# Performance work log

Measured on AMD Instinct MI355X. Metric: run time of the kernel, lower is better.

The kernel has to match this reference:

```python
import jax, jax.numpy as jnp
import numpy as np
import math

V, D, H, NL, L, B = 32000, 1024, 16, 6, 1024, 2
HD = D // H
EPS = 1e-5


def _positional(L, D):
    # matches torch: exp(arange(0,D,2) * -(log(1000)/D))
    div = jnp.exp(jnp.arange(0, D, 2, dtype=jnp.float32) * (-math.log(1000.0) / D))
    k = jnp.arange(L, dtype=jnp.float32)[:, None]
    pos = jnp.zeros((L, D), dtype=jnp.float32)
    pos = pos.at[:, 0::2].set(jnp.sin(k * div))
    pos = pos.at[:, 1::2].set(jnp.cos(k * div))
    return pos[None]  # [1, L, D]


def setup_inputs() -> dict:
    key = jax.random.key(0)
    ks = jax.random.split(key, 12)
    s = 0.02
    tokens = jax.random.randint(ks[0], (B, L), 0, V)
    emb = jax.random.normal(ks[1], (V, D), jnp.float32) * s
    pos = _positional(L, D)
    ln1_g = jnp.ones((NL, D), jnp.float32)
    ln1_b = jnp.zeros((NL, D), jnp.float32)
    ln2_g = jnp.ones((NL, D), jnp.float32)
    ln2_b = jnp.zeros((NL, D), jnp.float32)
    attn_w = jax.random.normal(ks[2], (NL, D, 3 * D), jnp.float32) * s
    attn_b = jnp.zeros((NL, 3 * D), jnp.float32)
    proj_w = jax.random.normal(ks[3], (NL, D, D), jnp.float32) * s
    proj_b = jnp.zeros((NL, D), jnp.float32)
    mlp_w1 = jax.random.normal(ks[4], (NL, D, 4 * D), jnp.float32) * s
    mlp_b1 = jnp.zeros((NL, 4 * D), jnp.float32)
    mlp_w2 = jax.random.normal(ks[5], (NL, 4 * D, D), jnp.float32) * s
    mlp_b2 = jnp.zeros((NL, D), jnp.float32)
    out_w = jax.random.normal(ks[6], (D, V), jnp.float32) * s
    return dict(tokens=tokens, pos=pos, emb=emb,
                ln1_g=ln1_g, ln1_b=ln1_b, ln2_g=ln2_g, ln2_b=ln2_b,
                attn_w=attn_w, attn_b=attn_b, proj_w=proj_w, proj_b=proj_b,
                mlp_w1=mlp_w1, mlp_b1=mlp_b1, mlp_w2=mlp_w2, mlp_b2=mlp_b2,
                out_w=out_w)


def _ln(x, g, b):
    mu = jnp.mean(x, -1, keepdims=True)
    var = jnp.mean(jnp.square(x - mu), -1, keepdims=True)
    return (x - mu) * jax.lax.rsqrt(var + EPS) * g + b


def _block(x, p, causal_mask):
    ln1_g, ln1_b, ln2_g, ln2_b, aw, ab, pw, pb, w1, b1, w2, b2 = p
    h = _ln(x, ln1_g, ln1_b)
    qkv = h @ aw + ab                      # [B, L, 3D]
    q, k, v = jnp.split(qkv, 3, axis=-1)
    Bc, Lc = x.shape[0], x.shape[1]
    q = q.reshape(Bc, Lc, H, HD)
    k = k.reshape(Bc, Lc, H, HD)
    v = v.reshape(Bc, Lc, H, HD)
    scores = jnp.einsum('blhd,bmhd->bhlm', q, k) * (1.0 / math.sqrt(HD))
    scores = jnp.where(causal_mask, scores, -jnp.inf)
    attn = jax.nn.softmax(scores, axis=-1)
    y = jnp.einsum('bhlm,bmhd->blhd', attn, v).reshape(Bc, Lc, D)
    x = x + (y @ pw + pb)
    r = _ln(x, ln2_g, ln2_b)
    # NOTE: original ModuleList order applies GELU AFTER the second linear
    r = jax.nn.gelu((r @ w1 + b1) @ w2 + b2, approximate=False)
    return x + r


def reference(tokens, pos, emb, ln1_g, ln1_b, ln2_g, ln2_b,
              attn_w, attn_b, proj_w, proj_b,
              mlp_w1, mlp_b1, mlp_w2, mlp_b2, out_w):
    x = emb[tokens] + pos                  # [B, L, D]
    Lc = x.shape[1]
    causal_mask = jnp.tril(jnp.ones((Lc, Lc), bool))[None, None]
    for i in range(NL):
        p = (ln1_g[i], ln1_b[i], ln2_g[i], ln2_b[i],
             attn_w[i], attn_b[i], proj_w[i], proj_b[i],
             mlp_w1[i], mlp_b1[i], mlp_w2[i], mlp_b2[i])
        x = _block(x, p, causal_mask)
    return x @ out_w                       # [B, L, V] logits
```

## Files before the change

### kernel.cpp

```cpp
#include <hip/hip_runtime.h>
#include <hip/hip_bf16.h>
#include <math.h>

typedef __bf16 bf16;
typedef __bf16 bf16x4 __attribute__((ext_vector_type(4)));
typedef __bf16 bf16x8 __attribute__((ext_vector_type(8)));
typedef float f32x4 __attribute__((ext_vector_type(4)));

__device__ __forceinline__ void gld_lds16(const void* g, void* l) {
    __builtin_amdgcn_global_load_lds(
        (const __attribute__((address_space(1))) unsigned int*)g,
        (__attribute__((address_space(3))) unsigned int*)l, 16, 0, 0);
}

#define VMW(n) asm volatile("s_waitcnt vmcnt(" #n ")" ::: "memory")
#define BARR() asm volatile("s_barrier" ::: "memory")

__global__ __launch_bounds__(256) void k_embed(const int* __restrict__ tok,
                                               const float* __restrict__ emb,
                                               const float* __restrict__ pos,
                                               float* __restrict__ x) {
    int row = blockIdx.x;
    int l = row & 1023;
    int tk = tok[row];
    const float4* e = (const float4*)(emb + (size_t)tk * 1024);
    const float4* p = (const float4*)(pos + (size_t)l * 1024);
    float4* o = (float4*)(x + (size_t)row * 1024);
    float4 a = e[threadIdx.x], b = p[threadIdx.x];
    o[threadIdx.x] = make_float4(a.x + b.x, a.y + b.y, a.z + b.z, a.w + b.w);
}

__global__ __launch_bounds__(256) void k_ln(const float* __restrict__ x,
                                            const float* __restrict__ g,
                                            const float* __restrict__ b,
                                            bf16* __restrict__ out) {
    int row = blockIdx.x;
    int t = threadIdx.x;
    const float4* xr = (const float4*)(x + (size_t)row * 1024);
    float4 v = xr[t];
    float s1 = v.x + v.y + v.z + v.w;
    float s2 = v.x * v.x + v.y * v.y + v.z * v.z + v.w * v.w;
#pragma unroll
    for (int o = 32; o; o >>= 1) { s1 += __shfl_down(s1, o); s2 += __shfl_down(s2, o); }
    __shared__ float ps1[4], ps2[4], stat[2];
    int lane = t & 63, wid = t >> 6;
    if (lane == 0) { ps1[wid] = s1; ps2[wid] = s2; }
    __syncthreads();
    if (t == 0) {
        float a1 = ps1[0] + ps1[1] + ps1[2] + ps1[3];
        float a2 = ps2[0] + ps2[1] + ps2[2] + ps2[3];
        float mu = a1 * (1.f / 1024.f);
        float var = a2 * (1.f / 1024.f) - mu * mu;
        stat[0] = mu; stat[1] = rsqrtf(var + 1e-5f);
    }
    __syncthreads();
    float mu = stat[0], rs = stat[1];
    const float4* gv = (const float4*)g;
    const float4* bv = (const float4*)b;
    float4 gg = gv[t], bb = bv[t];
    bf16x4 o4;
    o4[0] = (bf16)((v.x - mu) * rs * gg.x + bb.x);
    o4[1] = (bf16)((v.y - mu) * rs * gg.y + bb.y);
    o4[2] = (bf16)((v.z - mu) * rs * gg.z + bb.z);
    o4[3] = (bf16)((v.w - mu) * rs * gg.w + bb.w);
    *(bf16x4*)(out + (size_t)row * 1024 + t * 4) = o4;
}

__device__ __forceinline__ void transpose64(const float* __restrict__ W,
                                            bf16* __restrict__ WT,
                                            int K, int N, int n0, int k0, int t,
                                            float (*tile)[65]) {
    int tx = t & 15, ty = t >> 4;
#pragma unroll
    for (int i = 0; i < 64; i += 16) {
        float4 v = *(const float4*)&W[(size_t)(k0 + ty + i) * N + n0 + tx * 4];
        tile[ty + i][tx * 4 + 0] = v.x;
        tile[ty + i][tx * 4 + 1] = v.y;
        tile[ty + i][tx * 4 + 2] = v.z;
        tile[ty + i][tx * 4 + 3] = v.w;
    }
    __syncthreads();
    int n = t >> 3, ks = t & 7;
#pragma unroll
    for (int pass = 0; pass < 2; ++pass) {
        int nn = n + pass * 32;
        bf16x8 v;
#pragma unroll
        for (int j = 0; j < 8; ++j) v[j] = (bf16)tile[ks * 8 + j][nn];
        *(bf16x8*)&WT[(size_t)(n0 + nn) * K + k0 + ks * 8] = v;
    }
}

__device__ __forceinline__ void tr_layer_block(int bid,
                                               const float* aw, const float* pw,
                                               const float* m1, const float* m2,
                                               bf16* wT, int t, float (*tile)[65]) {
    const float* src; bf16* dst; int K, N, tn, tk;
    if (bid < 768)       { src = aw; dst = wT;            K = 1024; N = 3072; tn = bid % 48; tk = bid / 48; }
    else if (bid < 1024) { int b = bid - 768;  src = pw; dst = wT + 3145728; K = 1024; N = 1024; tn = b % 16; tk = b / 16; }
    else if (bid < 2048) { int b = bid - 1024; src = m1; dst = wT + 4194304; K = 1024; N = 4096; tn = b % 64; tk = b / 64; }
    else                 { int b = bid - 2048; src = m2; dst = wT + 8388608; K = 4096; N = 1024; tn = b % 16; tk = b / 16; }
    transpose64(src, dst, K, N, tn * 64, tk * 64, t, tile);
}

__global__ __launch_bounds__(256) void k_transpose_layer(const float* __restrict__ aw,
                                                         const float* __restrict__ pw,
                                                         const float* __restrict__ m1,
                                                         const float* __restrict__ m2,
                                                         bf16* __restrict__ wT) {
    __shared__ float tile[64][65];
    tr_layer_block(blockIdx.x, aw, pw, m1, m2, wT, threadIdx.x, tile);
}

__device__ __forceinline__ void stage128(const char* Ab, const char* Bb,
                                         char* As, char* Bs, int Kb, int k0b, int t) {
#pragma unroll
    for (int j = 0; j < 4; ++j) {
        int idx = j * 256 + t;
        int row = idx >> 3;
        int cb = (idx & 7) << 4;
        int scb = cb ^ ((row & 7) << 4);
        gld_lds16(Ab + (size_t)row * Kb + k0b + scb, As + idx * 16);
        gld_lds16(Bb + (size_t)row * Kb + k0b + scb, Bs + idx * 16);
    }
}

template <int EPI>
__global__ __launch_bounds__(256) void k_gemm2(const bf16* __restrict__ A,
                                               const bf16* __restrict__ BT,
                                               const float* __restrict__ bias,
                                               const float* __restrict__ resid,
                                               float* __restrict__ outf,
                                               bf16* __restrict__ outb,
                                               int N, int K) {
    __shared__ __align__(16) bf16 As[2][128 * 64];
    __shared__ __align__(16) bf16 Bs[2][128 * 64];
    int per = gridDim.x >> 3;
    int tile = (blockIdx.x & 7) * per + (blockIdx.x >> 3);
    int bm = tile & 15, bn = tile >> 4;
    int t = threadIdx.x, lane = t & 63;
    int wr = t >> 7, wc = (t >> 6) & 1;
    f32x4 acc[4][4] = {};
    const char* Ab = (const char*)(A + (size_t)bm * 128 * K);
    const char* Bb = (const char*)(BT + (size_t)bn * 128 * K);
    int Kb = K * 2;
    int nk = K >> 6;
    stage128(Ab, Bb, (char*)As[0], (char*)Bs[0], Kb, 0, t);
    VMW(0); BARR();
    for (int tt = 0; tt < nk; ++tt) {
        int cur = tt & 1;
        if (tt + 1 < nk)
            stage128(Ab, Bb, (char*)As[cur ^ 1], (char*)Bs[cur ^ 1], Kb, (tt + 1) * 128, t);
        const char* Ac = (const char*)As[cur];
        const char* Bc = (const char*)Bs[cur];
#pragma unroll
        for (int kk = 0; kk < 2; ++kk) {
            bf16x8 af[4], bfr[4];
            int cb = kk * 64 + ((lane >> 4) << 4);
#pragma unroll
            for (int m = 0; m < 4; ++m) {
                int r = wr * 64 + m * 16 + (lane & 15);
                af[m] = *(const bf16x8*)(Ac + r * 128 + (cb ^ ((r & 7) << 4)));
            }
#pragma unroll
            for (int n = 0; n < 4; ++n) {
                int r = wc * 64 + n * 16 + (lane & 15);
                bfr[n] = *(const bf16x8*)(Bc + r * 128 + (cb ^ ((r & 7) << 4)));
            }
#pragma unroll
            for (int m = 0; m < 4; ++m)
#pragma unroll
                for (int n = 0; n < 4; ++n)
                    acc[m][n] = __builtin_amdgcn_mfma_f32_16x16x32_bf16(af[m], bfr[n], acc[m][n], 0, 0, 0);
        }
        VMW(0); BARR();
    }
    int row0 = bm * 128 + wr * 64 + ((lane >> 4) << 2);
    int col0 = bn * 128 + wc * 64 + (lane & 15);
#pragma unroll
    for (int m = 0; m < 4; ++m) {
#pragma unroll
        for (int n = 0; n < 4; ++n) {
            int col = col0 + n * 16;
            float bv = bias[col];
#pragma unroll
            for (int r = 0; r < 4; ++r) {
                int row = row0 + m * 16 + r;
                size_t idx = (size_t)row * N + col;
                float v = acc[m][n][r] + bv;
                if (EPI == 0) {
                    outb[idx] = (bf16)v;
                } else if (EPI == 1) {
                    outf[idx] = resid[idx] + v;
                } else {
                    outf[idx] = resid[idx] + 0.5f * v * (1.0f + erff(v * 0.70710678118f));
                }
            }
        }
    }
}

__device__ __forceinline__ void stage64(const char* Ab, const char* Bb,
                                        char* As, char* Bs, int Kb, int k0b, int t) {
#pragma unroll
    for (int j = 0; j < 2; ++j) {
        int idx = j * 256 + t;
        int row = idx >> 3;
        int cb = (idx & 7) << 4;
        int scb = cb ^ ((row & 7) << 4);
        gld_lds16(Ab + (size_t)row * Kb + k0b + scb, As + idx * 16);
        gld_lds16(Bb + (size_t)row * Kb + k0b + scb, Bs + idx * 16);
    }
}

template <int EPI>
__global__ __launch_bounds__(256) void k_gemm64(const bf16* __restrict__ A,
                                                const bf16* __restrict__ BT,
                                                const float* __restrict__ bias,
                                                const float* __restrict__ resid,
                                                float* __restrict__ outf,
                                                bf16* __restrict__ outb,
                                                int N, int K) {
    __shared__ __align__(16) bf16 As[2][64 * 64];
    __shared__ __align__(16) bf16 Bs[2][64 * 64];
    int per = gridDim.x >> 3;
    int tile = (blockIdx.x & 7) * per + (blockIdx.x >> 3);
    int bm = tile & 31, bn = tile >> 5;
    int t = threadIdx.x, lane = t & 63, wid = t >> 6;
    f32x4 acc[4] = {};
    const char* Ab = (const char*)(A + (size_t)bm * 64 * K);
    const char* Bb = (const char*)(BT + (size_t)bn * 64 * K);
    int Kb = K * 2;
    int nk = K >> 6;
    stage64(Ab, Bb, (char*)As[0], (char*)Bs[0], Kb, 0, t);
    VMW(0); BARR();
    for (int tt = 0; tt < nk; ++tt) {
        int cur = tt & 1;
        if (tt + 1 < nk)
            stage64(Ab, Bb, (char*)As[cur ^ 1], (char*)Bs[cur ^ 1], Kb, (tt + 1) * 128, t);
        const char* Ac = (const char*)As[cur];
        const char* Bc = (const char*)Bs[cur];
#pragma unroll
        for (int kk = 0; kk < 2; ++kk) {
            int cb = kk * 64 + ((lane >> 4) << 4);
            int ra = wid * 16 + (lane & 15);
            bf16x8 af = *(const bf16x8*)(Ac + ra * 128 + (cb ^ ((ra & 7) << 4)));
            bf16x8 bfr[4];
#pragma unroll
            for (int n = 0; n < 4; ++n) {
                int r = n * 16 + (lane & 15);
                bfr[n] = *(const bf16x8*)(Bc + r * 128 + (cb ^ ((r & 7) << 4)));
            }
#pragma unroll
            for (int n = 0; n < 4; ++n)
                acc[n] = __builtin_amdgcn_mfma_f32_16x16x32_bf16(af, bfr[n], acc[n], 0, 0, 0);
        }
        VMW(0); BARR();
    }
    int row0 = bm * 64 + wid * 16 + ((lane >> 4) << 2);
    int col0 = bn * 64 + (lane & 15);
#pragma unroll
    for (int n = 0; n < 4; ++n) {
        int col = col0 + n * 16;
        float bv = bias[col];
#pragma unroll
        for (int r = 0; r < 4; ++r) {
            int row = row0 + r;
            size_t idx = (size_t)row * N + col;
            float v = acc[n][r] + bv;
            float res;
            if (EPI == 1) {
                res = resid[idx] + v;
            } else {
                res = resid[idx] + 0.5f * v * (1.0f + erff(v * 0.70710678118f));
            }
            outf[idx] = res;
            if (outb) outb[idx] = (bf16)res;
        }
    }
}

__device__ __forceinline__ void stage_full256(const char* gtile, char* ldst,
                                              int Kb, int t) {
#pragma unroll
    for (int j = 0; j < 4; ++j) {
        int idx = j * 512 + t;
        int row = idx >> 3;
        int cb = (idx & 7) << 4;
        int scb = cb ^ ((row & 7) << 4);
        gld_lds16(gtile + (size_t)row * Kb + scb, ldst + idx * 16);
    }
}

__device__ __forceinline__ void stage_half256(const char* gtile, char* ldst,
                                              int Kb, int t, int half) {
#pragma unroll
    for (int j = 0; j < 2; ++j) {
        int idx = (half * 2 + j) * 512 + t;
        int row = idx >> 3;
        int cb = (idx & 7) << 4;
        int scb = cb ^ ((row & 7) << 4);
        gld_lds16(gtile + (size_t)row * Kb + scb, ldst + idx * 16);
    }
}

template <int MH, int NH>
__device__ __forceinline__ void phase_rd(const char* Ac, const char* Bc,
                                         int lrow, int lk, int wm, int wn,
                                         bf16x8 (&af)[4][2], bf16x8 (&bfr)[2][2]) {
#pragma unroll
    for (int kk = 0; kk < 2; ++kk) {
        int cb = kk * 64 + lk * 16;
#pragma unroll
        for (int m = 0; m < 4; ++m) {
            int row = (MH * 4 + m) * 32 + wm * 16 + lrow;
            af[m][kk] = *(const bf16x8*)(Ac + row * 128 + (cb ^ ((row & 7) << 4)));
        }
#pragma unroll
        for (int n = 0; n < 2; ++n) {
            int row = (NH * 2 + n) * 64 + wn * 16 + lrow;
            bfr[n][kk] = *(const bf16x8*)(Bc + row * 128 + (cb ^ ((row & 7) << 4)));
        }
    }
}

template <int MH, int NH>
__device__ __forceinline__ void phase_mm(bf16x8 (&af)[4][2], bf16x8 (&bfr)[2][2],
                                         f32x4 (&acc)[8][4]) {
    __builtin_amdgcn_s_setprio(1);
#pragma unroll
    for (int kk = 0; kk < 2; ++kk)
#pragma unroll
        for (int m = 0; m < 4; ++m)
#pragma unroll
            for (int n = 0; n < 2; ++n)
                acc[MH * 4 + m][NH * 2 + n] = __builtin_amdgcn_mfma_f32_16x16x32_bf16(
                    af[m][kk], bfr[n][kk], acc[MH * 4 + m][NH * 2 + n], 0, 0, 0);
    __builtin_amdgcn_s_setprio(0);
    __builtin_amdgcn_sched_barrier(0);
}

__global__ __launch_bounds__(512, 1) void k_gemm256(const bf16* __restrict__ A,
                                                    const bf16* __restrict__ BT,
                                                    float* __restrict__ outf,
                                                    int N, int K) {
    __shared__ __align__(16) bf16 Asb[2][256 * 64];
    __shared__ __align__(16) bf16 Bsb[3][256 * 64];
    int t = threadIdx.x, lane = t & 63, wid = t >> 6;
    int wm = wid >> 2, wn = wid & 3;
    int lrow = lane & 15, lk = lane >> 4;
    int tile = (blockIdx.x & 7) * 125 + (blockIdx.x >> 3);
    int bm = tile & 7;
    int bn = tile >> 3;

    const char* Ab = (const char*)(A + (size_t)bm * 256 * K);
    const char* Bb = (const char*)(BT + (size_t)bn * 256 * K);
    int Kb = K * 2;
    int nk = K >> 6;
    f32x4 acc[8][4] = {};

    stage_full256(Ab, (char*)Asb[0], Kb, t);
    stage_full256(Bb, (char*)Bsb[0], Kb, t);
    stage_full256(Bb + 128, (char*)Bsb[1], Kb, t);

    for (int tt = 0; tt < nk; ++tt) {
        int ka = (tt + 1 < nk) ? tt + 1 : nk - 1;
        int kb = (tt + 2 < nk) ? tt + 2 : nk - 1;
        const char* Ac = (const char*)Asb[tt & 1];
        const char* Bc = (const char*)Bsb[tt % 3];
        char* An = (char*)Asb[(tt + 1) & 1];
        char* Bn = (char*)Bsb[(tt + 2) % 3];
        const char* Ag = Ab + (size_t)ka * 128;
        const char* Bg = Bb + (size_t)kb * 128;
        VMW(4); BARR();
        bf16x8 af[4][2], bfr[2][2];
        phase_rd<0, 0>(Ac, Bc, lrow, lk, wm, wn, af, bfr);
        stage_half256(Ag, An, Kb, t, 0);
        BARR();
        phase_mm<0, 0>(af, bfr, acc);
        BARR();
        phase_rd<0, 1>(Ac, Bc, lrow, lk, wm, wn, af, bfr);
        stage_half256(Ag, An, Kb, t, 1);
        BARR();
        phase_mm<0, 1>(af, bfr, acc);
        BARR();
        phase_rd<1, 0>(Ac, Bc, lrow, lk, wm, wn, af, bfr);
        stage_half256(Bg, Bn, Kb, t, 0);
        BARR();
        phase_mm<1, 0>(af, bfr, acc);
        BARR();
        phase_rd<1, 1>(Ac, Bc, lrow, lk, wm, wn, af, bfr);
        stage_half256(Bg, Bn, Kb, t, 1);
        BARR();
        phase_mm<1, 1>(af, bfr, acc);
        BARR();
    }

    size_t row0 = (size_t)bm * 256 + wm * 16 + (lane >> 4) * 4;
    int col0 = bn * 256 + wn * 16 + (lane & 15);
#pragma unroll
    for (int mi = 0; mi < 8; ++mi) {
#pragma unroll
        for (int ni = 0; ni < 4; ++ni) {
            int col = col0 + ni * 64;
#pragma unroll
            for (int r = 0; r < 4; ++r) {
                size_t row = row0 + mi * 32 + r;
                outf[row * N + col] = acc[mi][ni][r];
            }
        }
    }
}

__global__ __launch_bounds__(256) void k_attn_tr(const bf16* __restrict__ qkv,
                                                 bf16* __restrict__ y,
                                                 const float* __restrict__ aw,
                                                 const float* __restrict__ pw,
                                                 const float* __restrict__ m1,
                                                 const float* __restrict__ m2,
                                                 bf16* __restrict__ wTnext,
                                                 const float* __restrict__ outw,
                                                 bf16* __restrict__ outT) {
    __shared__ __align__(16) char smem[32768];
    int bidg = blockIdx.x;
    int t = threadIdx.x;
    if (bidg >= 512) {
        int tb = bidg - 512;
        float (*tile)[65] = (float(*)[65])smem;
        if (aw) {
            tr_layer_block(tb, aw, pw, m1, m2, wTnext, t, tile);
        } else {
            int tn = tb % 500, tk = tb / 500;
            transpose64(outw, outT, 1024, 32000, tn * 64, tk * 64, t, tile);
        }
        return;
    }
    bf16* Qs = (bf16*)smem;
    bf16* Ks = Qs + 4096;
    bf16* Vt = Ks + 4096;
    bf16* Ps = Vt + 4096;
    int tile = (bidg & 7) * 64 + (bidg >> 3);
    int qb = tile & 15;
    int bh = tile >> 4;
    int b = bh >> 4, h = bh & 15;
    int lane = t & 63, wid = t >> 6;
    int lr = lane & 15, lk = lane >> 4;
    int tok0 = b << 10;
    int q0 = qb << 6;
    const char* qbase = (const char*)qkv;
#pragma unroll
    for (int j = 0; j < 2; ++j) {
        int off = (j * 256 + t) * 16;
        int row = off >> 7, colb = off & 127;
        int scb = colb ^ ((row & 7) << 4);
        gld_lds16(qbase + ((size_t)(tok0 + q0 + row) * 3072 + h * 64) * 2 + scb, (char*)Qs + off);
    }
    VMW(0);
    __syncthreads();
    int qrw = wid * 16 + lr;
    int qsw = (qrw & 7) << 4;
    bf16x8 aq0 = *(const bf16x8*)((const char*)Qs + qrw * 128 + ((lk * 16) ^ qsw));
    bf16x8 aq1 = *(const bf16x8*)((const char*)Qs + qrw * 128 + ((64 + lk * 16) ^ qsw));
    f32x4 o[4] = {};
    float mrun[4], lrun[4];
#pragma unroll
    for (int r = 0; r < 4; ++r) { mrun[r] = -INFINITY; lrun[r] = 0.f; }
    int qrow = q0 + wid * 16 + lk * 4;

    for (int kv0 = 0; kv0 <= q0; kv0 += 64) {
        __syncthreads();
#pragma unroll
        for (int j = 0; j < 2; ++j) {
            int off = (j * 256 + t) * 16;
            int row = off >> 7, colb = off & 127;
            int scb = colb ^ ((row & 7) << 4);
            gld_lds16(qbase + ((size_t)(tok0 + kv0 + row) * 3072 + 1024 + h * 64) * 2 + scb,
                      (char*)Ks + off);
        }
        {
            int kv = t >> 2, d0 = (t & 3) * 16;
            const bf16* vrow = qkv + (size_t)(tok0 + kv0 + kv) * 3072 + 2048 + h * 64 + d0;
#pragma unroll
            for (int e4 = 0; e4 < 4; ++e4) {
                bf16x4 vv = *(const bf16x4*)(vrow + e4 * 4);
#pragma unroll
                for (int i = 0; i < 4; ++i) {
                    int d = d0 + e4 * 4 + i;
                    Vt[d * 64 + (kv ^ ((d & 7) << 3))] = vv[i];
                }
            }
        }
        VMW(0);
        __syncthreads();
        f32x4 s[4];
#pragma unroll
        for (int n = 0; n < 4; ++n) {
            int krw = n * 16 + lr;
            int ksw = (krw & 7) << 4;
            const char* kb = (const char*)Ks + krw * 128;
            bf16x8 bk0 = *(const bf16x8*)(kb + ((lk * 16) ^ ksw));
            bf16x8 bk1 = *(const bf16x8*)(kb + ((64 + lk * 16) ^ ksw));
            f32x4 z = {};
            z = __builtin_amdgcn_mfma_f32_16x16x32_bf16(aq0, bk0, z, 0, 0, 0);
            z = __builtin_amdgcn_mfma_f32_16x16x32_bf16(aq1, bk1, z, 0, 0, 0);
            s[n] = z;
        }
        float mx[4];
#pragma unroll
        for (int r = 0; r < 4; ++r) mx[r] = -INFINITY;
#pragma unroll
        for (int n = 0; n < 4; ++n) {
            int col = kv0 + n * 16 + lr;
#pragma unroll
            for (int r = 0; r < 4; ++r) {
                float sv = s[n][r] * 0.125f;
                sv = (col <= qrow + r) ? sv : -INFINITY;
                s[n][r] = sv;
                mx[r] = fmaxf(mx[r], sv);
            }
        }
#pragma unroll
        for (int r = 0; r < 4; ++r)
#pragma unroll
            for (int m = 1; m < 16; m <<= 1) mx[r] = fmaxf(mx[r], __shfl_xor(mx[r], m));
        float scl[4];
#pragma unroll
        for (int r = 0; r < 4; ++r) {
            float mn = fmaxf(mrun[r], mx[r]);
            scl[r] = __expf(mrun[r] - mn);
            mrun[r] = mn;
        }
        float rs[4] = {0.f, 0.f, 0.f, 0.f};
#pragma unroll
        for (int n = 0; n < 4; ++n)
#pragma unroll
            for (int r = 0; r < 4; ++r) {
                float p = __expf(s[n][r] - mrun[r]);
                s[n][r] = p;
                rs[r] += p;
            }
#pragma unroll
        for (int r = 0; r < 4; ++r) {
#pragma unroll
            for (int m = 1; m < 16; m <<= 1) rs[r] += __shfl_xor(rs[r], m);
            lrun[r] = lrun[r] * scl[r] + rs[r];
        }
#pragma unroll
        for (int n = 0; n < 4; ++n)
#pragma unroll
            for (int r = 0; r < 4; ++r) {
                o[n][r] *= scl[r];
                int prow = lk * 4 + r;
                Ps[wid * 1024 + prow * 64 + ((n * 16 + lr) ^ ((prow & 7) << 3))] = (bf16)s[n][r];
            }
        int psw = (lr & 7) << 3;
        const bf16* pb = Ps + wid * 1024 + lr * 64;
        bf16x8 ap0 = *(const bf16x8*)(pb + ((lk * 8) ^ psw));
        bf16x8 ap1 = *(const bf16x8*)(pb + ((32 + lk * 8) ^ psw));
#pragma unroll
        for (int n = 0; n < 4; ++n) {
            int vrw = n * 16 + lr;
            int vsw = (vrw & 7) << 3;
            const bf16* vb = Vt + vrw * 64;
            bf16x8 bv0 = *(const bf16x8*)(vb + ((lk * 8) ^ vsw));
            bf16x8 bv1 = *(const bf16x8*)(vb + ((32 + lk * 8) ^ vsw));
            o[n] = __builtin_amdgcn_mfma_f32_16x16x32_bf16(ap0, bv0, o[n], 0, 0, 0);
            o[n] = __builtin_amdgcn_mfma_f32_16x16x32_bf16(ap1, bv1, o[n], 0, 0, 0);
        }
    }
#pragma unroll
    for (int n = 0; n < 4; ++n)
#pragma unroll
        for (int r = 0; r < 4; ++r) {
            int row = tok0 + qrow + r;
            y[(size_t)row * 1024 + h * 64 + n * 16 + lr] = (bf16)(o[n][r] / lrun[r]);
        }
}

extern "C" void kernel_launch(void* const* d_in, const int* in_sizes, int n_in,
                              void* d_out, int out_size, void* d_ws, size_t ws_size,
                              hipStream_t stream) {
    const int*   tokens = (const int*)d_in[0];
    const float* pos    = (const float*)d_in[1];
    const float* emb    = (const float*)d_in[2];
    const float* ln1_g  = (const float*)d_in[3];
    const float* ln1_b  = (const float*)d_in[4];
    const float* ln2_g  = (const float*)d_in[5];
    const float* ln2_b  = (const float*)d_in[6];
    const float* attn_w = (const float*)d_in[7];
    const float* attn_b = (const float*)d_in[8];
    const float* proj_w = (const float*)d_in[9];
    const float* proj_b = (const float*)d_in[10];
    const float* mlp_w1 = (const float*)d_in[11];
    const float* mlp_b1 = (const float*)d_in[12];
    const float* mlp_w2 = (const float*)d_in[13];
    const float* mlp_b2 = (const float*)d_in[14];
    const float* out_w  = (const float*)d_in[15];
    float* out = (float*)d_out;

    char* ws = (char*)d_ws;
    size_t off = 0;
    auto alloc = [&](size_t bytes) {
        void* p = ws + off;
        off = (off + bytes + 255) & ~(size_t)255;
        return p;
    };
    float* x   = (float*)alloc((size_t)2048 * 1024 * 4);
    bf16* hb   = (bf16*)alloc((size_t)2048 * 1024 * 2);
    bf16* qkvb = (bf16*)alloc((size_t)2048 * 3072 * 2);
    bf16* yb   = (bf16*)alloc((size_t)2048 * 1024 * 2);
    bf16* hidb = (bf16*)alloc((size_t)2048 * 4096 * 2);
    bf16* outT = (bf16*)alloc((size_t)32000 * 1024 * 2);
    bf16* slot1 = (bf16*)alloc((size_t)9437184 * 2);
    bf16* slots[2] = { outT, slot1 };

    k_embed<<<2048, 256, 0, stream>>>(tokens, emb, pos, x);
    k_transpose_layer<<<3072, 256, 0, stream>>>(attn_w, proj_w, mlp_w1, mlp_w2, slots[0]);

    for (int i = 0; i < 6; ++i) {
        bf16* wT = slots[i & 1];
        k_ln<<<2048, 256, 0, stream>>>(x, ln1_g + i * 1024, ln1_b + i * 1024, hb);
        k_gemm2<0><<<384, 256, 0, stream>>>(hb, wT, attn_b + i * 3072,
                                            nullptr, nullptr, qkvb, 3072, 1024);
        if (i < 5) {
            int j = i + 1;
            k_attn_tr<<<3584, 256, 0, stream>>>(qkvb, yb,
                attn_w + (size_t)j * 1024 * 3072, proj_w + (size_t)j * 1024 * 1024,
                mlp_w1 + (size_t)j * 1024 * 4096, mlp_w2 + (size_t)j * 4096 * 1024,
                slots[j & 1], nullptr, nullptr);
        } else {
            k_attn_tr<<<8512, 256, 0, stream>>>(qkvb, yb,
                nullptr, nullptr, nullptr, nullptr, nullptr, out_w, outT);
        }
        k_gemm64<1><<<512, 256, 0, stream>>>(yb, wT + 3145728, proj_b + i * 1024,
                                             x, x, nullptr, 1024, 1024);
        k_ln<<<2048, 256, 0, stream>>>(x, ln2_g + i * 1024, ln2_b + i * 1024, hb);
        k_gemm2<0><<<512, 256, 0, stream>>>(hb, wT + 4194304, mlp_b1 + i * 4096,
                                            nullptr, nullptr, hidb, 4096, 1024);
        k_gemm64<2><<<512, 256, 0, stream>>>(hidb, wT + 8388608, mlp_b2 + i * 1024,
                                             x, x, (i == 5) ? hb : nullptr, 1024, 4096);
    }

    k_gemm256<<<1000, 512, 0, stream>>>(hb, outT, out, 32000, 1024);
}
```

Measured before the change: 1.137 ms.

## Replace 256-tile LM-head GEMM with 128-tile kernel and QKV with 64-tile GEMM

Removes the hand-pipelined 256x256 k_gemm256 kernel and computes the final vocab projection with the generic 128x128 k_gemm2, using a new no-bias fp32-output epilogue. The QKV projection moves from the 128-tile GEMM to the 64-tile GEMM, which gains a bf16-output epilogue, so it launches more blocks. This trades the LM head's larger tile and better operand reuse for simpler code, and gives the QKV GEMM more parallelism across CUs at the cost of more operand reloads.

```diff
diff --git a/kernel.cpp b/kernel.cpp
--- a/kernel.cpp
+++ b/kernel.cpp
@@ -182,7 +182,7 @@
 #pragma unroll
         for (int n = 0; n < 4; ++n) {
             int col = col0 + n * 16;
-            float bv = bias[col];
+            float bv = (EPI == 3) ? 0.f : bias[col];
 #pragma unroll
             for (int r = 0; r < 4; ++r) {
                 int row = row0 + m * 16 + r;
@@ -192,8 +192,10 @@
                     outb[idx] = (bf16)v;
                 } else if (EPI == 1) {
                     outf[idx] = resid[idx] + v;
+                } else if (EPI == 2) {
+                    outf[idx] = resid[idx] + 0.5f * v * (1.0f + erff(v * 0.70710678118f));
                 } else {
-                    outf[idx] = resid[idx] + 0.5f * v * (1.0f + erff(v * 0.70710678118f));
+                    outf[idx] = v;
                 }
             }
         }
@@ -268,145 +270,17 @@
             int row = row0 + r;
             size_t idx = (size_t)row * N + col;
             float v = acc[n][r] + bv;
-            float res;
-            if (EPI == 1) {
-                res = resid[idx] + v;
+            if (EPI == 0) {
+                outb[idx] = (bf16)v;
             } else {
-                res = resid[idx] + 0.5f * v * (1.0f + erff(v * 0.70710678118f));
-            }
-            outf[idx] = res;
-            if (outb) outb[idx] = (bf16)res;
-        }
-    }
-}
-
-__device__ __forceinline__ void stage_full256(const char* gtile, char* ldst,
-                                              int Kb, int t) {
-#pragma unroll
-    for (int j = 0; j < 4; ++j) {
-        int idx = j * 512 + t;
-        int row = idx >> 3;
-        int cb = (idx & 7) << 4;
-        int scb = cb ^ ((row & 7) << 4);
-        gld_lds16(gtile + (size_t)row * Kb + scb, ldst + idx * 16);
-    }
-}
-
-__device__ __forceinline__ void stage_half256(const char* gtile, char* ldst,
-                                              int Kb, int t, int half) {
-#pragma unroll
-    for (int j = 0; j < 2; ++j) {
-        int idx = (half * 2 + j) * 512 + t;
-        int row = idx >> 3;
-        int cb = (idx & 7) << 4;
-        int scb = cb ^ ((row & 7) << 4);
-        gld_lds16(gtile + (size_t)row * Kb + scb, ldst + idx * 16);
-    }
-}
-
-template <int MH, int NH>
-__device__ __forceinline__ void phase_rd(const char* Ac, const char* Bc,
-                                         int lrow, int lk, int wm, int wn,
-                                         bf16x8 (&af)[4][2], bf16x8 (&bfr)[2][2]) {
-#pragma unroll
-    for (int kk = 0; kk < 2; ++kk) {
-        int cb = kk * 64 + lk * 16;
-#pragma unroll
-        for (int m = 0; m < 4; ++m) {
-            int row = (MH * 4 + m) * 32 + wm * 16 + lrow;
-            af[m][kk] = *(const bf16x8*)(Ac + row * 128 + (cb ^ ((row & 7) << 4)));
-        }
-#pragma unroll
-        for (int n = 0; n < 2; ++n) {
-            int row = (NH * 2 + n) * 64 + wn * 16 + lrow;
-            bfr[n][kk] = *(const bf16x8*)(Bc + row * 128 + (cb ^ ((row & 7) << 4)));
-        }
-    }
-}
-
-template <int MH, int NH>
-__device__ __forceinline__ void phase_mm(bf16x8 (&af)[4][2], bf16x8 (&bfr)[2][2],
-                                         f32x4 (&acc)[8][4]) {
-    __builtin_amdgcn_s_setprio(1);
-#pragma unroll
-    for (int kk = 0; kk < 2; ++kk)
-#pragma unroll
-        for (int m = 0; m < 4; ++m)
-#pragma unroll
-            for (int n = 0; n < 2; ++n)
-                acc[MH * 4 + m][NH * 2 + n] = __builtin_amdgcn_mfma_f32_16x16x32_bf16(
-                    af[m][kk], bfr[n][kk], acc[MH * 4 + m][NH * 2 + n], 0, 0, 0);
-    __builtin_amdgcn_s_setprio(0);
-    __builtin_amdgcn_sched_barrier(0);
-}
-
-__global__ __launch_bounds__(512, 1) void k_gemm256(const bf16* __restrict__ A,
-                                                    const bf16* __restrict__ BT,
-                                                    float* __restrict__ outf,
-                                                    int N, int K) {
-    __shared__ __align__(16) bf16 Asb[2][256 * 64];
-    __shared__ __align__(16) bf16 Bsb[3][256 * 64];
-    int t = threadIdx.x, lane = t & 63, wid = t >> 6;
-    int wm = wid >> 2, wn = wid & 3;
-    int lrow = lane & 15, lk = lane >> 4;
-    int tile = (blockIdx.x & 7) * 125 + (blockIdx.x >> 3);
-    int bm = tile & 7;
-    int bn = tile >> 3;
-
-    const char* Ab = (const char*)(A + (size_t)bm * 256 * K);
-    const char* Bb = (const char*)(BT + (size_t)bn * 256 * K);
-    int Kb = K * 2;
-    int nk = K >> 6;
-    f32x4 acc[8][4] = {};
-
-    stage_full256(Ab, (char*)Asb[0], Kb, t);
-    stage_full256(Bb, (char*)Bsb[0], Kb, t);
-    stage_full256(Bb + 128, (char*)Bsb[1], Kb, t);
-
-    for (int tt = 0; tt < nk; ++tt) {
-        int ka = (tt + 1 < nk) ? tt + 1 : nk - 1;
-        int kb = (tt + 2 < nk) ? tt + 2 : nk - 1;
-        const char* Ac = (const char*)Asb[tt & 1];
-        const char* Bc = (const char*)Bsb[tt % 3];
-        char* An = (char*)Asb[(tt + 1) & 1];
-        char* Bn = (char*)Bsb[(tt + 2) % 3];
-        const char* Ag = Ab + (size_t)ka * 128;
-        const char* Bg = Bb + (size_t)kb * 128;
-        VMW(4); BARR();
-        bf16x8 af[4][2], bfr[2][2];
-        phase_rd<0, 0>(Ac, Bc, lrow, lk, wm, wn, af, bfr);
-        stage_half256(Ag, An, Kb, t, 0);
-        BARR();
-        phase_mm<0, 0>(af, bfr, acc);
-        BARR();
-        phase_rd<0, 1>(Ac, Bc, lrow, lk, wm, wn, af, bfr);
-        stage_half256(Ag, An, Kb, t, 1);
-        BARR();
-        phase_mm<0, 1>(af, bfr, acc);
-        BARR();
-        phase_rd<1, 0>(Ac, Bc, lrow, lk, wm, wn, af, bfr);
-        stage_half256(Bg, Bn, Kb, t, 0);
-        BARR();
-        phase_mm<1, 0>(af, bfr, acc);
-        BARR();
-        phase_rd<1, 1>(Ac, Bc, lrow, lk, wm, wn, af, bfr);
-        stage_half256(Bg, Bn, Kb, t, 1);
-        BARR();
-        phase_mm<1, 1>(af, bfr, acc);
-        BARR();
-    }
-
-    size_t row0 = (size_t)bm * 256 + wm * 16 + (lane >> 4) * 4;
-    int col0 = bn * 256 + wn * 16 + (lane & 15);
-#pragma unroll
-    for (int mi = 0; mi < 8; ++mi) {
-#pragma unroll
-        for (int ni = 0; ni < 4; ++ni) {
-            int col = col0 + ni * 64;
-#pragma unroll
-            for (int r = 0; r < 4; ++r) {
-                size_t row = row0 + mi * 32 + r;
-                outf[row * N + col] = acc[mi][ni][r];
+                float res;
+                if (EPI == 1) {
+                    res = resid[idx] + v;
+                } else {
+                    res = resid[idx] + 0.5f * v * (1.0f + erff(v * 0.70710678118f));
+                }
+                outf[idx] = res;
+                if (outb) outb[idx] = (bf16)res;
             }
         }
     }
@@ -620,8 +494,8 @@
     for (int i = 0; i < 6; ++i) {
         bf16* wT = slots[i & 1];
         k_ln<<<2048, 256, 0, stream>>>(x, ln1_g + i * 1024, ln1_b + i * 1024, hb);
-        k_gemm2<0><<<384, 256, 0, stream>>>(hb, wT, attn_b + i * 3072,
-                                            nullptr, nullptr, qkvb, 3072, 1024);
+        k_gemm64<0><<<1536, 256, 0, stream>>>(hb, wT, attn_b + i * 3072,
+                                              nullptr, nullptr, qkvb, 3072, 1024);
         if (i < 5) {
             int j = i + 1;
             k_attn_tr<<<3584, 256, 0, stream>>>(qkvb, yb,
@@ -641,5 +515,6 @@
                                              x, x, (i == 5) ? hb : nullptr, 1024, 4096);
     }
 
-    k_gemm256<<<1000, 512, 0, stream>>>(hb, outT, out, 32000, 1024);
-}
+    k_gemm2<3><<<4000, 256, 0, stream>>>(hb, outT, nullptr, nullptr, out, nullptr,
+                                         32000, 1024);
+}
```

After: 1.196 ms. 5.2% more time.

## Double-buffer K/V tiles in attention to overlap loads with compute

Applied to the files above, without the earlier changes.

Splits the K and transposed-V shared-memory buffers into two halves each. The next KV tile is prefetched while the current one is being computed: K goes through global-to-LDS loads and V through registers, and V is written to LDS after the PV MFMAs. This also removes one barrier per iteration. The goal is to hide global load latency in the attention kernel, at the cost of raising LDS use from 32KB to 48KB per block, which could lower occupancy. The attention kernel is only part of the total runtime.

```diff
diff --git a/kernel.cpp b/kernel.cpp
--- a/kernel.cpp
+++ b/kernel.cpp
@@ -421,7 +421,7 @@
                                                  bf16* __restrict__ wTnext,
                                                  const float* __restrict__ outw,
                                                  bf16* __restrict__ outT) {
-    __shared__ __align__(16) char smem[32768];
+    __shared__ __align__(16) char smem[49152];
     int bidg = blockIdx.x;
     int t = threadIdx.x;
     if (bidg >= 512) {
@@ -435,10 +435,12 @@
         }
         return;
     }
-    bf16* Qs = (bf16*)smem;
-    bf16* Ks = Qs + 4096;
-    bf16* Vt = Ks + 4096;
-    bf16* Ps = Vt + 4096;
+    bf16* Qs  = (bf16*)smem;
+    bf16* KsA = Qs + 4096;
+    bf16* KsB = KsA + 4096;
+    bf16* VtA = KsB + 4096;
+    bf16* VtB = VtA + 4096;
+    bf16* Ps  = VtB + 4096;
     int tile = (bidg & 7) * 64 + (bidg >> 3);
     int qb = tile & 15;
     int bh = tile >> 4;
@@ -448,6 +450,34 @@
     int tok0 = b << 10;
     int q0 = qb << 6;
     const char* qbase = (const char*)qkv;
+    int kvr = t >> 2, d0v = (t & 3) * 16;
+
+    auto stageK = [&](int kv0, bf16* Kb) {
+#pragma unroll
+        for (int j = 0; j < 2; ++j) {
+            int off = (j * 256 + t) * 16;
+            int row = off >> 7, colb = off & 127;
+            int scb = colb ^ ((row & 7) << 4);
+            gld_lds16(qbase + ((size_t)(tok0 + kv0 + row) * 3072 + 1024 + h * 64) * 2 + scb,
+                      (char*)Kb + off);
+        }
+    };
+    bf16x4 vreg[4];
+    auto loadV = [&](int kv0) {
+        const bf16* vrow = qkv + (size_t)(tok0 + kv0 + kvr) * 3072 + 2048 + h * 64 + d0v;
+#pragma unroll
+        for (int e4 = 0; e4 < 4; ++e4) vreg[e4] = *(const bf16x4*)(vrow + e4 * 4);
+    };
+    auto writeV = [&](bf16* Vb) {
+#pragma unroll
+        for (int e4 = 0; e4 < 4; ++e4)
+#pragma unroll
+            for (int i2 = 0; i2 < 4; ++i2) {
+                int d = d0v + e4 * 4 + i2;
+                Vb[d * 64 + (kvr ^ ((d & 7) << 3))] = vreg[e4][i2];
+            }
+    };
+
 #pragma unroll
     for (int j = 0; j < 2; ++j) {
         int off = (j * 256 + t) * 16;
@@ -455,8 +485,12 @@
         int scb = colb ^ ((row & 7) << 4);
         gld_lds16(qbase + ((size_t)(tok0 + q0 + row) * 3072 + h * 64) * 2 + scb, (char*)Qs + off);
     }
+    stageK(0, KsA);
+    loadV(0);
     VMW(0);
+    writeV(VtA);
     __syncthreads();
+
     int qrw = wid * 16 + lr;
     int qsw = (qrw & 7) << 4;
     bf16x8 aq0 = *(const bf16x8*)((const char*)Qs + qrw * 128 + ((lk * 16) ^ qsw));
@@ -466,38 +500,22 @@
 #pragma unroll
     for (int r = 0; r < 4; ++r) { mrun[r] = -INFINITY; lrun[r] = 0.f; }
     int qrow = q0 + wid * 16 + lk * 4;
-
-    for (int kv0 = 0; kv0 <= q0; kv0 += 64) {
-        __syncthreads();
-#pragma unroll
-        for (int j = 0; j < 2; ++j) {
-            int off = (j * 256 + t) * 16;
-            int row = off >> 7, colb = off & 127;
-            int scb = colb ^ ((row & 7) << 4);
-            gld_lds16(qbase + ((size_t)(tok0 + kv0 + row) * 3072 + 1024 + h * 64) * 2 + scb,
-                      (char*)Ks + off);
-        }
-        {
-            int kv = t >> 2, d0 = (t & 3) * 16;
-            const bf16* vrow = qkv + (size_t)(tok0 + kv0 + kv) * 3072 + 2048 + h * 64 + d0;
-#pragma unroll
-            for (int e4 = 0; e4 < 4; ++e4) {
-                bf16x4 vv = *(const bf16x4*)(vrow + e4 * 4);
-#pragma unroll
-                for (int i = 0; i < 4; ++i) {
-                    int d = d0 + e4 * 4 + i;
-                    Vt[d * 64 + (kv ^ ((d & 7) << 3))] = vv[i];
-                }
-            }
-        }
-        VMW(0);
-        __syncthreads();
+    int nt = qb + 1;
+
+    for (int ti = 0; ti < nt; ++ti) {
+        int kv0 = ti << 6;
+        bf16* Kc = (ti & 1) ? KsB : KsA;
+        bf16* Vc = (ti & 1) ? VtB : VtA;
+        bf16* Kn = (ti & 1) ? KsA : KsB;
+        bf16* Vn = (ti & 1) ? VtA : VtB;
+        bool pf = (ti + 1 < nt);
+        if (pf) { stageK((ti + 1) << 6, Kn); loadV((ti + 1) << 6); }
         f32x4 s[4];
 #pragma unroll
         for (int n = 0; n < 4; ++n) {
             int krw = n * 16 + lr;
             int ksw = (krw & 7) << 4;
-            const char* kb = (const char*)Ks + krw * 128;
+            const char* kb = (const char*)Kc + krw * 128;
             bf16x8 bk0 = *(const bf16x8*)(kb + ((lk * 16) ^ ksw));
             bf16x8 bk1 = *(const bf16x8*)(kb + ((64 + lk * 16) ^ ksw));
             f32x4 z = {};
@@ -561,12 +579,14 @@
         for (int n = 0; n < 4; ++n) {
             int vrw = n * 16 + lr;
             int vsw = (vrw & 7) << 3;
-            const bf16* vb = Vt + vrw * 64;
+            const bf16* vb = Vc + vrw * 64;
             bf16x8 bv0 = *(const bf16x8*)(vb + ((lk * 8) ^ vsw));
             bf16x8 bv1 = *(const bf16x8*)(vb + ((32 + lk * 8) ^ vsw));
             o[n] = __builtin_amdgcn_mfma_f32_16x16x32_bf16(ap0, bv0, o[n], 0, 0, 0);
             o[n] = __builtin_amdgcn_mfma_f32_16x16x32_bf16(ap1, bv1, o[n], 0, 0, 0);
         }
+        if (pf) { VMW(0); writeV(Vn); }
+        __syncthreads();
     }
 #pragma unroll
     for (int n = 0; n < 4; ++n)
```

Measured after the change: 1.132 ms. No clear change (-0.5%).
